# Optimization experiments

Hardware: AMD Instinct MI355X
Metric: run time of the kernel (lower is better)

The kernel has to match this reference:

```python
import jax, jax.numpy as jnp
import numpy as np

MAX_DEPTH = 83.0
PI = 3.1415926535
SCALE = 8
FOCAL = 715.0

def setup_inputs() -> dict:
    key = jax.random.key(0)
    ks = jax.random.split(key, 16)
    B, C, H, W = 16, 128, 44, 152
    x = jax.random.normal(ks[0], (B, C, H, W), dtype=jnp.float32)
    # reduction 1x1 convs: 128->64->32->16->8->4
    chans = [128, 64, 32, 16, 8, 4]
    inp = {"x": x}
    for i in range(5):
        cin, cout = chans[i], chans[i + 1]
        w = jax.random.normal(ks[1 + 2 * i], (cout, cin), dtype=jnp.float32) * (1.0 / np.sqrt(cin))
        b = jax.random.normal(ks[2 + 2 * i], (cout,), dtype=jnp.float32) * 0.01
        inp[f"w{i}"] = w
        inp[f"b{i}"] = b
    # final 1x1 conv: 4 -> 3
    inp["cw"] = jax.random.normal(ks[11], (3, 4), dtype=jnp.float32) * 0.5
    inp["cb"] = jax.random.normal(ks[12], (3,), dtype=jnp.float32) * 0.01
    return inp

def _lpg_block(x, w0, b0, w1, b1, w2, b2, w3, b3, w4, b4, cw, cb):
    # reduction chain: 1x1 conv + ELU
    for w, b in ((w0, b0), (w1, b1), (w2, b2), (w3, b3), (w4, b4)):
        x = jax.nn.elu(jnp.einsum('oc,bchw->bohw', w, x) + b[None, :, None, None])
    # 4 -> 3 conv producing (theta, phi, dist) logits
    y = jnp.einsum('oc,bchw->bohw', cw, x) + cb[None, :, None, None]
    theta = jax.nn.sigmoid(y[:, 0]) * PI / 6.0          # [B,H,W]
    phi = jax.nn.sigmoid(y[:, 1]) * PI * 2.0
    dist = jax.nn.sigmoid(y[:, 2]) * MAX_DEPTH
    n1 = jnp.sin(theta) * jnp.cos(phi)
    n2 = jnp.sin(theta) * jnp.sin(phi)
    n3 = jnp.cos(theta)
    n = jnp.stack([n1, n2, n3], axis=1)                  # [B,3,H,W]
    # F.normalize(p=2, dim=1, eps=1e-12)
    norm = jnp.sqrt(jnp.sum(n * n, axis=1, keepdims=True))
    n = n / jnp.maximum(norm, 1e-12)
    n1, n2, n3 = n[:, 0], n[:, 1], n[:, 2]
    # LPG expansion: depth[b, y*s+ii, x*s+jj] = dist / (n1*u[jj] + n2*v[ii] + n3)
    s = SCALE
    off = (jnp.arange(s, dtype=jnp.float32) - (s - 1) / 2.0) / s / FOCAL  # [s]
    v = off[:, None]   # rows (ii)
    u = off[None, :]   # cols (jj)
    denom = (n1[..., None, None] * u + n2[..., None, None] * v
             + n3[..., None, None])                       # [B,H,W,s,s]
    depth = dist[..., None, None] / denom                 # [B,H,W,s,s]
    B, H, W = dist.shape
    depth = jnp.transpose(depth, (0, 1, 3, 2, 4)).reshape(B, 1, H * s, W * s)
    return depth

def reference(x, w0, b0, w1, b1, w2, b2, w3, b3, w4, b4, cw, cb):
    return _lpg_block(x, w0, b0, w1, b1, w2, b2, w3, b3, w4, b4, cw, cb)
```

## Files before the change

kernel.cpp:

```cpp
#include <hip/hip_runtime.h>
#include <math.h>

#define HW_   6688
#define W_    152
#define NPIX  107008
#define OW_   1216
#define OHW_  428032

typedef _Float16 f16;
typedef _Float16 f16x2 __attribute__((ext_vector_type(2)));
typedef _Float16 f16x4 __attribute__((ext_vector_type(4)));
typedef _Float16 f16x8 __attribute__((ext_vector_type(8)));
typedef float    f32x4 __attribute__((ext_vector_type(4)));

#define MFMA(a,b,c) __builtin_amdgcn_mfma_f32_16x16x32_f16((a),(b),(c),0,0,0)

#define SXH_STR  72
#define SA1_OFF  0
#define SA1_STR  40
#define SA2_OFF  2560
#define SA2_STR  24
#define SA3_OFF  4096
#define SA3_STR  16
#define SA0_OFF  5120
#define SA0_STR  72
#define LDSF16   9728

__device__ __forceinline__ float fast_sigmoid(float v) {
    return __builtin_amdgcn_rcpf(1.0f + __expf(-v));
}
__device__ __forceinline__ float eluf(float v) {
    return v > 0.0f ? v : (__expf(v) - 1.0f);
}
__device__ __forceinline__ void split8(const float* v, f16x8& hi, f16x8& lo) {
#pragma unroll
    for (int e = 0; e < 8; ++e) {
        f16 h = (f16)v[e];
        hi[e] = h;
        lo[e] = (f16)(v[e] - (float)h);
    }
}
__device__ __forceinline__ f16x8 cvt8h(const float* v) {
    f16x8 r;
#pragma unroll
    for (int e = 0; e < 8; ++e) r[e] = (f16)v[e];
    return r;
}
__device__ __forceinline__ f16x4 elu_cvt4(f32x4 a) {
    f16x4 r;
    r[0] = (f16)eluf(a[0]); r[1] = (f16)eluf(a[1]);
    r[2] = (f16)eluf(a[2]); r[3] = (f16)eluf(a[3]);
    return r;
}
__device__ __forceinline__ void wave_fence() {
    __builtin_amdgcn_sched_barrier(0);
    __builtin_amdgcn_wave_barrier();
    __builtin_amdgcn_sched_barrier(0);
}

__global__ __launch_bounds__(256, 6)
void lpg_mfma(const float* __restrict__ x,
              const float* __restrict__ w0, const float* __restrict__ b0,
              const float* __restrict__ w1, const float* __restrict__ b1,
              const float* __restrict__ w2, const float* __restrict__ b2,
              const float* __restrict__ w3, const float* __restrict__ b3,
              const float* __restrict__ w4, const float* __restrict__ b4,
              const float* __restrict__ cw, const float* __restrict__ cb,
              float* __restrict__ out) {
    __shared__ __align__(16) f16 S[LDSF16];

    const int tid  = threadIdx.x;
    const int wv   = __builtin_amdgcn_readfirstlane(tid >> 6);
    const int lane = tid & 63;
    const int p    = lane & 15;
    const int q    = lane >> 4;
    const int pixbase = blockIdx.x * 64;

    const int i    = tid & 63;
    const int csub = (tid >> 6) * 16;
    int pixs = pixbase + i;
    int bbs  = pixs / HW_;
    int hws  = pixs - bbs * HW_;
    const float* xps = x + ((size_t)bbs * 128 + csub) * HW_ + hws;
    f16* dsts = S + i * SXH_STR + csub;

#pragma unroll 8
    for (int k = 0; k < 16; k += 2) {
        float v0 = xps[(size_t)k * HW_];
        float v1 = xps[(size_t)(k + 1) * HW_];
        auto pk = __builtin_amdgcn_cvt_pkrtz(v0, v1);
        f16x2 h; h[0] = (f16)pk[0]; h[1] = (f16)pk[1];
        *(f16x2*)(dsts + k) = h;
    }

    const int w0row = (wv * 16 + p) * 128 + q * 8;
    f16x8 w0h[2], w0l[2];
#pragma unroll
    for (int kt = 0; kt < 2; ++kt) {
        float v[8];
#pragma unroll
        for (int e = 0; e < 8; ++e) v[e] = w0[w0row + kt * 32 + e];
        split8(v, w0h[kt], w0l[kt]);
    }
    f32x4 acc[4];
    {
        f32x4 b0v = *(const f32x4*)(b0 + wv * 16 + 4 * q);
#pragma unroll
        for (int t = 0; t < 4; ++t) acc[t] = b0v;
    }
    __syncthreads();

#pragma unroll 2
    for (int t = 0; t < 4; ++t) {
        const f16* bp = S + (t * 16 + p) * SXH_STR + q * 8;
        f16x8 bf0 = *(const f16x8*)(bp);
        f16x8 bf1 = *(const f16x8*)(bp + 32);
        acc[t] = MFMA(w0h[0], bf0, acc[t]); acc[t] = MFMA(w0l[0], bf0, acc[t]);
        acc[t] = MFMA(w0h[1], bf1, acc[t]); acc[t] = MFMA(w0l[1], bf1, acc[t]);
    }
    __syncthreads();

#pragma unroll 8
    for (int k = 0; k < 16; k += 2) {
        float v0 = xps[(size_t)(k + 64) * HW_];
        float v1 = xps[(size_t)(k + 65) * HW_];
        auto pk = __builtin_amdgcn_cvt_pkrtz(v0, v1);
        f16x2 h; h[0] = (f16)pk[0]; h[1] = (f16)pk[1];
        *(f16x2*)(dsts + k) = h;
    }
#pragma unroll
    for (int kt = 0; kt < 2; ++kt) {
        float v[8];
#pragma unroll
        for (int e = 0; e < 8; ++e) v[e] = w0[w0row + 64 + kt * 32 + e];
        split8(v, w0h[kt], w0l[kt]);
    }
    __syncthreads();

#pragma unroll 2
    for (int t = 0; t < 4; ++t) {
        const f16* bp = S + (t * 16 + p) * SXH_STR + q * 8;
        f16x8 bf0 = *(const f16x8*)(bp);
        f16x8 bf1 = *(const f16x8*)(bp + 32);
        acc[t] = MFMA(w0h[0], bf0, acc[t]); acc[t] = MFMA(w0l[0], bf0, acc[t]);
        acc[t] = MFMA(w0h[1], bf1, acc[t]); acc[t] = MFMA(w0l[1], bf1, acc[t]);
        *(f16x4*)(S + SA0_OFF + (t * 16 + p) * SA0_STR + wv * 16 + 4 * q) = elu_cvt4(acc[t]);
    }
    __syncthreads();

    const f32x4 z4 = {0.f, 0.f, 0.f, 0.f};
    const int i0 = wv * 16 + p;

    {
        f16x8 wf[2][2];
#pragma unroll
        for (int Mt = 0; Mt < 2; ++Mt)
#pragma unroll
            for (int kt = 0; kt < 2; ++kt)
                wf[Mt][kt] = cvt8h(w1 + (Mt * 16 + p) * 64 + kt * 32 + q * 8);
        f32x4 c0 = *(const f32x4*)(b1 + 4 * q);
        f32x4 c1 = *(const f32x4*)(b1 + 16 + 4 * q);
#pragma unroll
        for (int kt = 0; kt < 2; ++kt) {
            f16x8 bf = *(const f16x8*)(S + SA0_OFF + i0 * SA0_STR + kt * 32 + q * 8);
            c0 = MFMA(wf[0][kt], bf, c0);
            c1 = MFMA(wf[1][kt], bf, c1);
        }
        *(f16x4*)(S + SA1_OFF + i0 * SA1_STR + 4 * q)      = elu_cvt4(c0);
        *(f16x4*)(S + SA1_OFF + i0 * SA1_STR + 16 + 4 * q) = elu_cvt4(c1);
    }
    wave_fence();

    {
        f16x8 wf = cvt8h(w2 + p * 32 + q * 8);
        f16x8 bf = *(const f16x8*)(S + SA1_OFF + i0 * SA1_STR + q * 8);
        f32x4 c = *(const f32x4*)(b2 + 4 * q);
        c = MFMA(wf, bf, c);
        *(f16x4*)(S + SA2_OFF + i0 * SA2_STR + 4 * q) = elu_cvt4(c);
    }
    wave_fence();

    {
        f16x8 wf = (f16x8){};
        if (p < 8 && q < 2) wf = cvt8h(w3 + p * 16 + q * 8);
        f16x8 bf = *(const f16x8*)(S + SA2_OFF + i0 * SA2_STR + (q & 1) * 8);
        f32x4 c = (q < 2) ? *(const f32x4*)(b3 + 4 * q) : z4;
        c = MFMA(wf, bf, c);
        if (q < 2) *(f16x4*)(S + SA3_OFF + i0 * SA3_STR + 4 * q) = elu_cvt4(c);
    }
    wave_fence();

    f32x4 cy;
    {
        f16x8 wf = (f16x8){};
        if (p < 4 && q == 0) wf = cvt8h(w4 + p * 8);
        f16x8 bf = *(const f16x8*)(S + SA3_OFF + i0 * SA3_STR);
        f32x4 c = (q == 0) ? *(const f32x4*)(b4) : z4;
        c = MFMA(wf, bf, c);

        f16x8 hh = (f16x8){};
        if (q == 0) {
#pragma unroll
            for (int e = 0; e < 4; ++e) hh[e] = (f16)eluf(c[e]);
        }
        f16x8 wh = (f16x8){};
        if (p < 3 && q == 0) {
#pragma unroll
            for (int e = 0; e < 4; ++e) wh[e] = (f16)cw[p * 4 + e];
        }
        cy = z4;
        if (q == 0) { cy[0] = cb[0]; cy[1] = cb[1]; cy[2] = cb[2]; }
        cy = MFMA(wh, hh, cy);
    }

    {
        float y0 = __shfl(cy[0], p);
        float y1 = __shfl(cy[1], p);
        float y2 = __shfl(cy[2], p);

        float theta = 0.5235987756f * fast_sigmoid(y0);
        float phi   = 6.2831853072f * fast_sigmoid(y1);
        float dist  = 83.0f         * fast_sigmoid(y2);
        float st = __sinf(theta), ct = __cosf(theta);
        float sp = __sinf(phi),   cp = __cosf(phi);
        float n1 = st * cp, n2 = st * sp, n3 = ct;
        float inv = __frsqrt_rn(fmaf(n1, n1, fmaf(n2, n2, n3 * n3)));
        n1 *= inv; n2 *= inv; n3 *= inv;

        const float ksc = 1.0f / (8.0f * 715.0f);
        float nu[8];
#pragma unroll
        for (int j = 0; j < 8; ++j) nu[j] = n1 * (((float)j - 3.5f) * ksc);

        int pix = pixbase + i0;
        int bb  = pix / HW_;
        int hw  = pix - bb * HW_;
        int hh  = hw / W_;
        int ww  = hw - hh * W_;
        const int obase = bb * OHW_ + (hh * 8) * OW_ + ww * 8;
#pragma unroll
        for (int r = 0; r < 2; ++r) {
            int irow = q * 2 + r;
            float base = fmaf(n2, ((float)irow - 3.5f) * ksc, n3);
            float4 r0, r1;
            r0.x = dist * __builtin_amdgcn_rcpf(base + nu[0]);
            r0.y = dist * __builtin_amdgcn_rcpf(base + nu[1]);
            r0.z = dist * __builtin_amdgcn_rcpf(base + nu[2]);
            r0.w = dist * __builtin_amdgcn_rcpf(base + nu[3]);
            r1.x = dist * __builtin_amdgcn_rcpf(base + nu[4]);
            r1.y = dist * __builtin_amdgcn_rcpf(base + nu[5]);
            r1.z = dist * __builtin_amdgcn_rcpf(base + nu[6]);
            r1.w = dist * __builtin_amdgcn_rcpf(base + nu[7]);
            float4* op = (float4*)(out + obase + irow * OW_);
            op[0] = r0;
            op[1] = r1;
        }
    }
}

extern "C" void kernel_launch(void* const* d_in, const int* in_sizes, int n_in,
                              void* d_out, int out_size, void* d_ws, size_t ws_size,
                              hipStream_t stream) {
    const float* x  = (const float*)d_in[0];
    const float* w0 = (const float*)d_in[1];
    const float* b0 = (const float*)d_in[2];
    const float* w1 = (const float*)d_in[3];
    const float* b1 = (const float*)d_in[4];
    const float* w2 = (const float*)d_in[5];
    const float* b2 = (const float*)d_in[6];
    const float* w3 = (const float*)d_in[7];
    const float* b3 = (const float*)d_in[8];
    const float* w4 = (const float*)d_in[9];
    const float* b4 = (const float*)d_in[10];
    const float* cw = (const float*)d_in[11];
    const float* cb = (const float*)d_in[12];
    float* outp = (float*)d_out;

    lpg_mfma<<<NPIX / 64, 256, 0, stream>>>(x, w0, b0, w1, b1, w2, b2, w3, b3,
                                            w4, b4, cw, cb, outp);
}
```

Baseline: 30.88 us.

## Split fused LPG kernel into layer-0 GEMM kernel and tail kernel via workspace

The single fused kernel is split in two. The first kernel loads all 128 input channels into LDS in one pass with a wider stride, runs the first 1x1 conv with split-precision MFMA, and writes the ELU activations as f16 to a global workspace. The second kernel reads those activations directly from global memory for the remaining reduction layers and the depth expansion. This removes the two-phase staging and extra barriers, and the second kernel uses less LDS. In exchange it adds a launch and a round trip of about 13.7 MB of f16 activations through global memory.

```diff
diff --git a/kernel.cpp b/kernel.cpp
--- a/kernel.cpp
+++ b/kernel.cpp
@@ -15,17 +15,6 @@
 
 #define MFMA(a,b,c) __builtin_amdgcn_mfma_f32_16x16x32_f16((a),(b),(c),0,0,0)
 
-#define SXH_STR  72
-#define SA1_OFF  0
-#define SA1_STR  40
-#define SA2_OFF  2560
-#define SA2_STR  24
-#define SA3_OFF  4096
-#define SA3_STR  16
-#define SA0_OFF  5120
-#define SA0_STR  72
-#define LDSF16   9728
-
 __device__ __forceinline__ float fast_sigmoid(float v) {
     return __builtin_amdgcn_rcpf(1.0f + __expf(-v));
 }
@@ -58,16 +47,81 @@
     __builtin_amdgcn_sched_barrier(0);
 }
 
+#define SX_STR 136
 __global__ __launch_bounds__(256, 6)
-void lpg_mfma(const float* __restrict__ x,
-              const float* __restrict__ w0, const float* __restrict__ b0,
+void lpg_l0(const float* __restrict__ x, const float* __restrict__ w0,
+            const float* __restrict__ b0, f16* __restrict__ a0) {
+    __shared__ __align__(16) f16 SX[64 * SX_STR];
+
+    const int tid  = threadIdx.x;
+    const int wv   = __builtin_amdgcn_readfirstlane(tid >> 6);
+    const int lane = tid & 63;
+    const int p    = lane & 15;
+    const int q    = lane >> 4;
+    const int pixbase = blockIdx.x * 64;
+
+    const int i    = tid & 63;
+    const int csub = (tid >> 6) * 32;
+    int pixs = pixbase + i;
+    int bbs  = pixs / HW_;
+    int hws  = pixs - bbs * HW_;
+    const float* xps = x + ((size_t)bbs * 128 + csub) * HW_ + hws;
+    f16* dsts = SX + i * SX_STR + csub;
+#pragma unroll 8
+    for (int k = 0; k < 32; k += 2) {
+        float v0 = xps[(size_t)k * HW_];
+        float v1 = xps[(size_t)(k + 1) * HW_];
+        auto pk = __builtin_amdgcn_cvt_pkrtz(v0, v1);
+        f16x2 h; h[0] = (f16)pk[0]; h[1] = (f16)pk[1];
+        *(f16x2*)(dsts + k) = h;
+    }
+
+    f32x4 acc[4];
+    {
+        f32x4 b0v = *(const f32x4*)(b0 + wv * 16 + 4 * q);
+#pragma unroll
+        for (int t = 0; t < 4; ++t) acc[t] = b0v;
+    }
+    const int w0row = (wv * 16 + p) * 128 + q * 8;
+
+    __syncthreads();
+
+#pragma unroll
+    for (int kt = 0; kt < 4; ++kt) {
+        float v[8];
+#pragma unroll
+        for (int e = 0; e < 8; ++e) v[e] = w0[w0row + kt * 32 + e];
+        f16x8 wh, wl; split8(v, wh, wl);
+#pragma unroll
+        for (int t = 0; t < 4; ++t) {
+            f16x8 bf = *(const f16x8*)(SX + (t * 16 + p) * SX_STR + kt * 32 + q * 8);
+            acc[t] = MFMA(wh, bf, acc[t]);
+            acc[t] = MFMA(wl, bf, acc[t]);
+        }
+    }
+#pragma unroll
+    for (int t = 0; t < 4; ++t)
+        *(f16x4*)(a0 + (size_t)(pixbase + t * 16 + p) * 64 + wv * 16 + 4 * q) =
+            elu_cvt4(acc[t]);
+}
+
+#define T_SA1_OFF 0
+#define T_SA1_STR 40
+#define T_SA2_OFF 2560
+#define T_SA2_STR 24
+#define T_SA3_OFF 4096
+#define T_SA3_STR 16
+#define T_LDSF16  5120
+
+__global__ __launch_bounds__(256, 6)
+void lpg_tail(const f16* __restrict__ a0,
               const float* __restrict__ w1, const float* __restrict__ b1,
               const float* __restrict__ w2, const float* __restrict__ b2,
               const float* __restrict__ w3, const float* __restrict__ b3,
               const float* __restrict__ w4, const float* __restrict__ b4,
               const float* __restrict__ cw, const float* __restrict__ cb,
               float* __restrict__ out) {
-    __shared__ __align__(16) f16 S[LDSF16];
+    __shared__ __align__(16) f16 S[T_LDSF16];
 
     const int tid  = threadIdx.x;
     const int wv   = __builtin_amdgcn_readfirstlane(tid >> 6);
@@ -75,83 +129,13 @@
     const int p    = lane & 15;
     const int q    = lane >> 4;
     const int pixbase = blockIdx.x * 64;
-
-    const int i    = tid & 63;
-    const int csub = (tid >> 6) * 16;
-    int pixs = pixbase + i;
-    int bbs  = pixs / HW_;
-    int hws  = pixs - bbs * HW_;
-    const float* xps = x + ((size_t)bbs * 128 + csub) * HW_ + hws;
-    f16* dsts = S + i * SXH_STR + csub;
-
-#pragma unroll 8
-    for (int k = 0; k < 16; k += 2) {
-        float v0 = xps[(size_t)k * HW_];
-        float v1 = xps[(size_t)(k + 1) * HW_];
-        auto pk = __builtin_amdgcn_cvt_pkrtz(v0, v1);
-        f16x2 h; h[0] = (f16)pk[0]; h[1] = (f16)pk[1];
-        *(f16x2*)(dsts + k) = h;
-    }
-
-    const int w0row = (wv * 16 + p) * 128 + q * 8;
-    f16x8 w0h[2], w0l[2];
-#pragma unroll
-    for (int kt = 0; kt < 2; ++kt) {
-        float v[8];
-#pragma unroll
-        for (int e = 0; e < 8; ++e) v[e] = w0[w0row + kt * 32 + e];
-        split8(v, w0h[kt], w0l[kt]);
-    }
-    f32x4 acc[4];
-    {
-        f32x4 b0v = *(const f32x4*)(b0 + wv * 16 + 4 * q);
-#pragma unroll
-        for (int t = 0; t < 4; ++t) acc[t] = b0v;
-    }
-    __syncthreads();
-
-#pragma unroll 2
-    for (int t = 0; t < 4; ++t) {
-        const f16* bp = S + (t * 16 + p) * SXH_STR + q * 8;
-        f16x8 bf0 = *(const f16x8*)(bp);
-        f16x8 bf1 = *(const f16x8*)(bp + 32);
-        acc[t] = MFMA(w0h[0], bf0, acc[t]); acc[t] = MFMA(w0l[0], bf0, acc[t]);
-        acc[t] = MFMA(w0h[1], bf1, acc[t]); acc[t] = MFMA(w0l[1], bf1, acc[t]);
-    }
-    __syncthreads();
-
-#pragma unroll 8
-    for (int k = 0; k < 16; k += 2) {
-        float v0 = xps[(size_t)(k + 64) * HW_];
-        float v1 = xps[(size_t)(k + 65) * HW_];
-        auto pk = __builtin_amdgcn_cvt_pkrtz(v0, v1);
-        f16x2 h; h[0] = (f16)pk[0]; h[1] = (f16)pk[1];
-        *(f16x2*)(dsts + k) = h;
-    }
-#pragma unroll
-    for (int kt = 0; kt < 2; ++kt) {
-        float v[8];
-#pragma unroll
-        for (int e = 0; e < 8; ++e) v[e] = w0[w0row + 64 + kt * 32 + e];
-        split8(v, w0h[kt], w0l[kt]);
-    }
-    __syncthreads();
-
-#pragma unroll 2
-    for (int t = 0; t < 4; ++t) {
-        const f16* bp = S + (t * 16 + p) * SXH_STR + q * 8;
-        f16x8 bf0 = *(const f16x8*)(bp);
-        f16x8 bf1 = *(const f16x8*)(bp + 32);
-        acc[t] = MFMA(w0h[0], bf0, acc[t]); acc[t] = MFMA(w0l[0], bf0, acc[t]);
-        acc[t] = MFMA(w0h[1], bf1, acc[t]); acc[t] = MFMA(w0l[1], bf1, acc[t]);
-        *(f16x4*)(S + SA0_OFF + (t * 16 + p) * SA0_STR + wv * 16 + 4 * q) = elu_cvt4(acc[t]);
-    }
-    __syncthreads();
-
     const f32x4 z4 = {0.f, 0.f, 0.f, 0.f};
     const int i0 = wv * 16 + p;
 
     {
+        const f16* arow = a0 + (size_t)(pixbase + i0) * 64;
+        f16x8 bf0 = *(const f16x8*)(arow + q * 8);
+        f16x8 bf1 = *(const f16x8*)(arow + 32 + q * 8);
         f16x8 wf[2][2];
 #pragma unroll
         for (int Mt = 0; Mt < 2; ++Mt)
@@ -160,33 +144,29 @@
                 wf[Mt][kt] = cvt8h(w1 + (Mt * 16 + p) * 64 + kt * 32 + q * 8);
         f32x4 c0 = *(const f32x4*)(b1 + 4 * q);
         f32x4 c1 = *(const f32x4*)(b1 + 16 + 4 * q);
-#pragma unroll
-        for (int kt = 0; kt < 2; ++kt) {
-            f16x8 bf = *(const f16x8*)(S + SA0_OFF + i0 * SA0_STR + kt * 32 + q * 8);
-            c0 = MFMA(wf[0][kt], bf, c0);
-            c1 = MFMA(wf[1][kt], bf, c1);
-        }
-        *(f16x4*)(S + SA1_OFF + i0 * SA1_STR + 4 * q)      = elu_cvt4(c0);
-        *(f16x4*)(S + SA1_OFF + i0 * SA1_STR + 16 + 4 * q) = elu_cvt4(c1);
+        c0 = MFMA(wf[0][0], bf0, c0); c0 = MFMA(wf[0][1], bf1, c0);
+        c1 = MFMA(wf[1][0], bf0, c1); c1 = MFMA(wf[1][1], bf1, c1);
+        *(f16x4*)(S + T_SA1_OFF + i0 * T_SA1_STR + 4 * q)      = elu_cvt4(c0);
+        *(f16x4*)(S + T_SA1_OFF + i0 * T_SA1_STR + 16 + 4 * q) = elu_cvt4(c1);
     }
     wave_fence();
 
     {
         f16x8 wf = cvt8h(w2 + p * 32 + q * 8);
-        f16x8 bf = *(const f16x8*)(S + SA1_OFF + i0 * SA1_STR + q * 8);
+        f16x8 bf = *(const f16x8*)(S + T_SA1_OFF + i0 * T_SA1_STR + q * 8);
         f32x4 c = *(const f32x4*)(b2 + 4 * q);
         c = MFMA(wf, bf, c);
-        *(f16x4*)(S + SA2_OFF + i0 * SA2_STR + 4 * q) = elu_cvt4(c);
+        *(f16x4*)(S + T_SA2_OFF + i0 * T_SA2_STR + 4 * q) = elu_cvt4(c);
     }
     wave_fence();
 
     {
         f16x8 wf = (f16x8){};
         if (p < 8 && q < 2) wf = cvt8h(w3 + p * 16 + q * 8);
-        f16x8 bf = *(const f16x8*)(S + SA2_OFF + i0 * SA2_STR + (q & 1) * 8);
+        f16x8 bf = *(const f16x8*)(S + T_SA2_OFF + i0 * T_SA2_STR + (q & 1) * 8);
         f32x4 c = (q < 2) ? *(const f32x4*)(b3 + 4 * q) : z4;
         c = MFMA(wf, bf, c);
-        if (q < 2) *(f16x4*)(S + SA3_OFF + i0 * SA3_STR + 4 * q) = elu_cvt4(c);
+        if (q < 2) *(f16x4*)(S + T_SA3_OFF + i0 * T_SA3_STR + 4 * q) = elu_cvt4(c);
     }
     wave_fence();
 
@@ -194,7 +174,7 @@
     {
         f16x8 wf = (f16x8){};
         if (p < 4 && q == 0) wf = cvt8h(w4 + p * 8);
-        f16x8 bf = *(const f16x8*)(S + SA3_OFF + i0 * SA3_STR);
+        f16x8 bf = *(const f16x8*)(S + T_SA3_OFF + i0 * T_SA3_STR);
         f32x4 c = (q == 0) ? *(const f32x4*)(b4) : z4;
         c = MFMA(wf, bf, c);
 
@@ -274,8 +254,10 @@
     const float* b4 = (const float*)d_in[10];
     const float* cw = (const float*)d_in[11];
     const float* cb = (const float*)d_in[12];
+    f16* a0    = (f16*)d_ws;
     float* outp = (float*)d_out;
 
-    lpg_mfma<<<NPIX / 64, 256, 0, stream>>>(x, w0, b0, w1, b1, w2, b2, w3, b3,
+    lpg_l0<<<NPIX / 64, 256, 0, stream>>>(x, w0, b0, a0);
+    lpg_tail<<<NPIX / 64, 256, 0, stream>>>(a0, w1, b1, w2, b2, w3, b3,
                                             w4, b4, cw, cb, outp);
 }
```

Result: slower. 40.00 us (+29.5%).

## Process two pixel tiles per block with register prefetch of next tile

Applied to the files above, without the earlier changes.

Each block now handles 128 pixels as two sequential 64-pixel tiles, loading the second tile's input channels into registers while the first tile runs its reduction chain and output stage. This is meant to overlap global load latency with MFMA and epilogue work and amortize per-block setup. It adds register pressure (32 extra floats per thread), an extra block barrier per tile, and halves the grid size, which may reduce latency hiding across CUs.

```diff
diff --git a/kernel.cpp b/kernel.cpp
--- a/kernel.cpp
+++ b/kernel.cpp
@@ -57,6 +57,14 @@
     __builtin_amdgcn_wave_barrier();
     __builtin_amdgcn_sched_barrier(0);
 }
+__device__ __forceinline__ void write16(const float (&v)[16], f16* dst) {
+#pragma unroll
+    for (int k = 0; k < 16; k += 2) {
+        auto pk = __builtin_amdgcn_cvt_pkrtz(v[k], v[k + 1]);
+        f16x2 h; h[0] = (f16)pk[0]; h[1] = (f16)pk[1];
+        *(f16x2*)(dst + k) = h;
+    }
+}
 
 __global__ __launch_bounds__(256, 6)
 void lpg_mfma(const float* __restrict__ x,
@@ -74,186 +82,198 @@
     const int lane = tid & 63;
     const int p    = lane & 15;
     const int q    = lane >> 4;
-    const int pixbase = blockIdx.x * 64;
+    const int pixbase0 = blockIdx.x * 128;
 
     const int i    = tid & 63;
     const int csub = (tid >> 6) * 16;
-    int pixs = pixbase + i;
-    int bbs  = pixs / HW_;
-    int hws  = pixs - bbs * HW_;
-    const float* xps = x + ((size_t)bbs * 128 + csub) * HW_ + hws;
     f16* dsts = S + i * SXH_STR + csub;
-
-#pragma unroll 8
-    for (int k = 0; k < 16; k += 2) {
-        float v0 = xps[(size_t)k * HW_];
-        float v1 = xps[(size_t)(k + 1) * HW_];
-        auto pk = __builtin_amdgcn_cvt_pkrtz(v0, v1);
-        f16x2 h; h[0] = (f16)pk[0]; h[1] = (f16)pk[1];
-        *(f16x2*)(dsts + k) = h;
-    }
-
     const int w0row = (wv * 16 + p) * 128 + q * 8;
-    f16x8 w0h[2], w0l[2];
-#pragma unroll
-    for (int kt = 0; kt < 2; ++kt) {
-        float v[8];
-#pragma unroll
-        for (int e = 0; e < 8; ++e) v[e] = w0[w0row + kt * 32 + e];
-        split8(v, w0h[kt], w0l[kt]);
-    }
-    f32x4 acc[4];
-    {
-        f32x4 b0v = *(const f32x4*)(b0 + wv * 16 + 4 * q);
-#pragma unroll
-        for (int t = 0; t < 4; ++t) acc[t] = b0v;
-    }
-    __syncthreads();
-
-#pragma unroll 2
-    for (int t = 0; t < 4; ++t) {
-        const f16* bp = S + (t * 16 + p) * SXH_STR + q * 8;
-        f16x8 bf0 = *(const f16x8*)(bp);
-        f16x8 bf1 = *(const f16x8*)(bp + 32);
-        acc[t] = MFMA(w0h[0], bf0, acc[t]); acc[t] = MFMA(w0l[0], bf0, acc[t]);
-        acc[t] = MFMA(w0h[1], bf1, acc[t]); acc[t] = MFMA(w0l[1], bf1, acc[t]);
-    }
-    __syncthreads();
-
-#pragma unroll 8
-    for (int k = 0; k < 16; k += 2) {
-        float v0 = xps[(size_t)(k + 64) * HW_];
-        float v1 = xps[(size_t)(k + 65) * HW_];
-        auto pk = __builtin_amdgcn_cvt_pkrtz(v0, v1);
-        f16x2 h; h[0] = (f16)pk[0]; h[1] = (f16)pk[1];
-        *(f16x2*)(dsts + k) = h;
-    }
-#pragma unroll
-    for (int kt = 0; kt < 2; ++kt) {
-        float v[8];
-#pragma unroll
-        for (int e = 0; e < 8; ++e) v[e] = w0[w0row + 64 + kt * 32 + e];
-        split8(v, w0h[kt], w0l[kt]);
-    }
-    __syncthreads();
-
-#pragma unroll 2
-    for (int t = 0; t < 4; ++t) {
-        const f16* bp = S + (t * 16 + p) * SXH_STR + q * 8;
-        f16x8 bf0 = *(const f16x8*)(bp);
-        f16x8 bf1 = *(const f16x8*)(bp + 32);
-        acc[t] = MFMA(w0h[0], bf0, acc[t]); acc[t] = MFMA(w0l[0], bf0, acc[t]);
-        acc[t] = MFMA(w0h[1], bf1, acc[t]); acc[t] = MFMA(w0l[1], bf1, acc[t]);
-        *(f16x4*)(S + SA0_OFF + (t * 16 + p) * SA0_STR + wv * 16 + 4 * q) = elu_cvt4(acc[t]);
-    }
-    __syncthreads();
-
     const f32x4 z4 = {0.f, 0.f, 0.f, 0.f};
     const int i0 = wv * 16 + p;
 
+    float vh0[16], vh1[16];
     {
-        f16x8 wf[2][2];
-#pragma unroll
-        for (int Mt = 0; Mt < 2; ++Mt)
-#pragma unroll
-            for (int kt = 0; kt < 2; ++kt)
-                wf[Mt][kt] = cvt8h(w1 + (Mt * 16 + p) * 64 + kt * 32 + q * 8);
-        f32x4 c0 = *(const f32x4*)(b1 + 4 * q);
-        f32x4 c1 = *(const f32x4*)(b1 + 16 + 4 * q);
+        int pixs = pixbase0 + i;
+        int bbs  = pixs / HW_;
+        int hws  = pixs - bbs * HW_;
+        const float* xp = x + ((size_t)bbs * 128 + csub) * HW_ + hws;
+#pragma unroll
+        for (int k = 0; k < 16; ++k) vh0[k] = xp[(size_t)k * HW_];
+#pragma unroll
+        for (int k = 0; k < 16; ++k) vh1[k] = xp[(size_t)(k + 64) * HW_];
+    }
+
+#pragma unroll
+    for (int tt = 0; tt < 2; ++tt) {
+        const int pixbase = pixbase0 + tt * 64;
+
+        write16(vh0, dsts);
+
+        f16x8 w0h[2], w0l[2];
 #pragma unroll
         for (int kt = 0; kt < 2; ++kt) {
-            f16x8 bf = *(const f16x8*)(S + SA0_OFF + i0 * SA0_STR + kt * 32 + q * 8);
-            c0 = MFMA(wf[0][kt], bf, c0);
-            c1 = MFMA(wf[1][kt], bf, c1);
-        }
-        *(f16x4*)(S + SA1_OFF + i0 * SA1_STR + 4 * q)      = elu_cvt4(c0);
-        *(f16x4*)(S + SA1_OFF + i0 * SA1_STR + 16 + 4 * q) = elu_cvt4(c1);
-    }
-    wave_fence();
-
-    {
-        f16x8 wf = cvt8h(w2 + p * 32 + q * 8);
-        f16x8 bf = *(const f16x8*)(S + SA1_OFF + i0 * SA1_STR + q * 8);
-        f32x4 c = *(const f32x4*)(b2 + 4 * q);
-        c = MFMA(wf, bf, c);
-        *(f16x4*)(S + SA2_OFF + i0 * SA2_STR + 4 * q) = elu_cvt4(c);
-    }
-    wave_fence();
-
-    {
-        f16x8 wf = (f16x8){};
-        if (p < 8 && q < 2) wf = cvt8h(w3 + p * 16 + q * 8);
-        f16x8 bf = *(const f16x8*)(S + SA2_OFF + i0 * SA2_STR + (q & 1) * 8);
-        f32x4 c = (q < 2) ? *(const f32x4*)(b3 + 4 * q) : z4;
-        c = MFMA(wf, bf, c);
-        if (q < 2) *(f16x4*)(S + SA3_OFF + i0 * SA3_STR + 4 * q) = elu_cvt4(c);
-    }
-    wave_fence();
-
-    f32x4 cy;
-    {
-        f16x8 wf = (f16x8){};
-        if (p < 4 && q == 0) wf = cvt8h(w4 + p * 8);
-        f16x8 bf = *(const f16x8*)(S + SA3_OFF + i0 * SA3_STR);
-        f32x4 c = (q == 0) ? *(const f32x4*)(b4) : z4;
-        c = MFMA(wf, bf, c);
-
-        f16x8 hh = (f16x8){};
-        if (q == 0) {
-#pragma unroll
-            for (int e = 0; e < 4; ++e) hh[e] = (f16)eluf(c[e]);
-        }
-        f16x8 wh = (f16x8){};
-        if (p < 3 && q == 0) {
-#pragma unroll
-            for (int e = 0; e < 4; ++e) wh[e] = (f16)cw[p * 4 + e];
-        }
-        cy = z4;
-        if (q == 0) { cy[0] = cb[0]; cy[1] = cb[1]; cy[2] = cb[2]; }
-        cy = MFMA(wh, hh, cy);
-    }
-
-    {
-        float y0 = __shfl(cy[0], p);
-        float y1 = __shfl(cy[1], p);
-        float y2 = __shfl(cy[2], p);
-
-        float theta = 0.5235987756f * fast_sigmoid(y0);
-        float phi   = 6.2831853072f * fast_sigmoid(y1);
-        float dist  = 83.0f         * fast_sigmoid(y2);
-        float st = __sinf(theta), ct = __cosf(theta);
-        float sp = __sinf(phi),   cp = __cosf(phi);
-        float n1 = st * cp, n2 = st * sp, n3 = ct;
-        float inv = __frsqrt_rn(fmaf(n1, n1, fmaf(n2, n2, n3 * n3)));
-        n1 *= inv; n2 *= inv; n3 *= inv;
-
-        const float ksc = 1.0f / (8.0f * 715.0f);
-        float nu[8];
-#pragma unroll
-        for (int j = 0; j < 8; ++j) nu[j] = n1 * (((float)j - 3.5f) * ksc);
-
-        int pix = pixbase + i0;
-        int bb  = pix / HW_;
-        int hw  = pix - bb * HW_;
-        int hh  = hw / W_;
-        int ww  = hw - hh * W_;
-        const int obase = bb * OHW_ + (hh * 8) * OW_ + ww * 8;
-#pragma unroll
-        for (int r = 0; r < 2; ++r) {
-            int irow = q * 2 + r;
-            float base = fmaf(n2, ((float)irow - 3.5f) * ksc, n3);
-            float4 r0, r1;
-            r0.x = dist * __builtin_amdgcn_rcpf(base + nu[0]);
-            r0.y = dist * __builtin_amdgcn_rcpf(base + nu[1]);
-            r0.z = dist * __builtin_amdgcn_rcpf(base + nu[2]);
-            r0.w = dist * __builtin_amdgcn_rcpf(base + nu[3]);
-            r1.x = dist * __builtin_amdgcn_rcpf(base + nu[4]);
-            r1.y = dist * __builtin_amdgcn_rcpf(base + nu[5]);
-            r1.z = dist * __builtin_amdgcn_rcpf(base + nu[6]);
-            r1.w = dist * __builtin_amdgcn_rcpf(base + nu[7]);
-            float4* op = (float4*)(out + obase + irow * OW_);
-            op[0] = r0;
-            op[1] = r1;
+            float v[8];
+#pragma unroll
+            for (int e = 0; e < 8; ++e) v[e] = w0[w0row + kt * 32 + e];
+            split8(v, w0h[kt], w0l[kt]);
+        }
+        f32x4 acc[4];
+        {
+            f32x4 b0v = *(const f32x4*)(b0 + wv * 16 + 4 * q);
+#pragma unroll
+            for (int t = 0; t < 4; ++t) acc[t] = b0v;
+        }
+        __syncthreads();
+
+#pragma unroll 2
+        for (int t = 0; t < 4; ++t) {
+            const f16* bp = S + (t * 16 + p) * SXH_STR + q * 8;
+            f16x8 bf0 = *(const f16x8*)(bp);
+            f16x8 bf1 = *(const f16x8*)(bp + 32);
+            acc[t] = MFMA(w0h[0], bf0, acc[t]); acc[t] = MFMA(w0l[0], bf0, acc[t]);
+            acc[t] = MFMA(w0h[1], bf1, acc[t]); acc[t] = MFMA(w0l[1], bf1, acc[t]);
+        }
+        __syncthreads();
+
+        write16(vh1, dsts);
+#pragma unroll
+        for (int kt = 0; kt < 2; ++kt) {
+            float v[8];
+#pragma unroll
+            for (int e = 0; e < 8; ++e) v[e] = w0[w0row + 64 + kt * 32 + e];
+            split8(v, w0h[kt], w0l[kt]);
+        }
+        __syncthreads();
+
+#pragma unroll 2
+        for (int t = 0; t < 4; ++t) {
+            const f16* bp = S + (t * 16 + p) * SXH_STR + q * 8;
+            f16x8 bf0 = *(const f16x8*)(bp);
+            f16x8 bf1 = *(const f16x8*)(bp + 32);
+            acc[t] = MFMA(w0h[0], bf0, acc[t]); acc[t] = MFMA(w0l[0], bf0, acc[t]);
+            acc[t] = MFMA(w0h[1], bf1, acc[t]); acc[t] = MFMA(w0l[1], bf1, acc[t]);
+            *(f16x4*)(S + SA0_OFF + (t * 16 + p) * SA0_STR + wv * 16 + 4 * q) =
+                elu_cvt4(acc[t]);
+        }
+        __syncthreads();
+
+        if (tt == 0) {
+            int pixs = pixbase0 + 64 + i;
+            int bbs  = pixs / HW_;
+            int hws  = pixs - bbs * HW_;
+            const float* xp = x + ((size_t)bbs * 128 + csub) * HW_ + hws;
+#pragma unroll
+            for (int k = 0; k < 16; ++k) vh0[k] = xp[(size_t)k * HW_];
+#pragma unroll
+            for (int k = 0; k < 16; ++k) vh1[k] = xp[(size_t)(k + 64) * HW_];
+        }
+
+        {
+            f16x8 wf[2][2];
+#pragma unroll
+            for (int Mt = 0; Mt < 2; ++Mt)
+#pragma unroll
+                for (int kt = 0; kt < 2; ++kt)
+                    wf[Mt][kt] = cvt8h(w1 + (Mt * 16 + p) * 64 + kt * 32 + q * 8);
+            f32x4 c0 = *(const f32x4*)(b1 + 4 * q);
+            f32x4 c1 = *(const f32x4*)(b1 + 16 + 4 * q);
+#pragma unroll
+            for (int kt = 0; kt < 2; ++kt) {
+                f16x8 bf = *(const f16x8*)(S + SA0_OFF + i0 * SA0_STR + kt * 32 + q * 8);
+                c0 = MFMA(wf[0][kt], bf, c0);
+                c1 = MFMA(wf[1][kt], bf, c1);
+            }
+            *(f16x4*)(S + SA1_OFF + i0 * SA1_STR + 4 * q)      = elu_cvt4(c0);
+            *(f16x4*)(S + SA1_OFF + i0 * SA1_STR + 16 + 4 * q) = elu_cvt4(c1);
+        }
+        wave_fence();
+
+        {
+            f16x8 wf = cvt8h(w2 + p * 32 + q * 8);
+            f16x8 bf = *(const f16x8*)(S + SA1_OFF + i0 * SA1_STR + q * 8);
+            f32x4 c = *(const f32x4*)(b2 + 4 * q);
+            c = MFMA(wf, bf, c);
+            *(f16x4*)(S + SA2_OFF + i0 * SA2_STR + 4 * q) = elu_cvt4(c);
+        }
+        wave_fence();
+
+        {
+            f16x8 wf = (f16x8){};
+            if (p < 8 && q < 2) wf = cvt8h(w3 + p * 16 + q * 8);
+            f16x8 bf = *(const f16x8*)(S + SA2_OFF + i0 * SA2_STR + (q & 1) * 8);
+            f32x4 c = (q < 2) ? *(const f32x4*)(b3 + 4 * q) : z4;
+            c = MFMA(wf, bf, c);
+            if (q < 2) *(f16x4*)(S + SA3_OFF + i0 * SA3_STR + 4 * q) = elu_cvt4(c);
+        }
+        wave_fence();
+
+        f32x4 cy;
+        {
+            f16x8 wf = (f16x8){};
+            if (p < 4 && q == 0) wf = cvt8h(w4 + p * 8);
+            f16x8 bf = *(const f16x8*)(S + SA3_OFF + i0 * SA3_STR);
+            f32x4 c = (q == 0) ? *(const f32x4*)(b4) : z4;
+            c = MFMA(wf, bf, c);
+
+            f16x8 hh = (f16x8){};
+            if (q == 0) {
+#pragma unroll
+                for (int e = 0; e < 4; ++e) hh[e] = (f16)eluf(c[e]);
+            }
+            f16x8 wh = (f16x8){};
+            if (p < 3 && q == 0) {
+#pragma unroll
+                for (int e = 0; e < 4; ++e) wh[e] = (f16)cw[p * 4 + e];
+            }
+            cy = z4;
+            if (q == 0) { cy[0] = cb[0]; cy[1] = cb[1]; cy[2] = cb[2]; }
+            cy = MFMA(wh, hh, cy);
+        }
+
+        __syncthreads();
+
+        {
+            float y0 = __shfl(cy[0], p);
+            float y1 = __shfl(cy[1], p);
+            float y2 = __shfl(cy[2], p);
+
+            float theta = 0.5235987756f * fast_sigmoid(y0);
+            float phi   = 6.2831853072f * fast_sigmoid(y1);
+            float dist  = 83.0f         * fast_sigmoid(y2);
+            float st = __sinf(theta), ct = __cosf(theta);
+            float sp = __sinf(phi),   cp = __cosf(phi);
+            float n1 = st * cp, n2 = st * sp, n3 = ct;
+            float inv = __frsqrt_rn(fmaf(n1, n1, fmaf(n2, n2, n3 * n3)));
+            n1 *= inv; n2 *= inv; n3 *= inv;
+
+            const float ksc = 1.0f / (8.0f * 715.0f);
+            float nu[8];
+#pragma unroll
+            for (int j = 0; j < 8; ++j) nu[j] = n1 * (((float)j - 3.5f) * ksc);
+
+            int pix = pixbase + i0;
+            int bb  = pix / HW_;
+            int hw  = pix - bb * HW_;
+            int hh  = hw / W_;
+            int ww  = hw - hh * W_;
+            const int obase = bb * OHW_ + (hh * 8) * OW_ + ww * 8;
+#pragma unroll
+            for (int r = 0; r < 2; ++r) {
+                int irow = q * 2 + r;
+                float base = fmaf(n2, ((float)irow - 3.5f) * ksc, n3);
+                float4 r0, r1;
+                r0.x = dist * __builtin_amdgcn_rcpf(base + nu[0]);
+                r0.y = dist * __builtin_amdgcn_rcpf(base + nu[1]);
+                r0.z = dist * __builtin_amdgcn_rcpf(base + nu[2]);
+                r0.w = dist * __builtin_amdgcn_rcpf(base + nu[3]);
+                r1.x = dist * __builtin_amdgcn_rcpf(base + nu[4]);
+                r1.y = dist * __builtin_amdgcn_rcpf(base + nu[5]);
+                r1.z = dist * __builtin_amdgcn_rcpf(base + nu[6]);
+                r1.w = dist * __builtin_amdgcn_rcpf(base + nu[7]);
+                float4* op = (float4*)(out + obase + irow * OW_);
+                op[0] = r0;
+                op[1] = r1;
+            }
         }
     }
 }
@@ -276,6 +296,6 @@
     const float* cb = (const float*)d_in[12];
     float* outp = (float*)d_out;
 
-    lpg_mfma<<<NPIX / 64, 256, 0, stream>>>(x, w0, b0, w1, b1, w2, b2, w3, b3,
-                                            w4, b4, cw, cb, outp);
-}
+    lpg_mfma<<<NPIX / 128, 256, 0, stream>>>(x, w0, b0, w1, b1, w2, b2, w3, b3,
+                                             w4, b4, cw, cb, outp);
+}
```

After: 42.91 us. 38.9% more time.
